# Kernel optimization log

Measured on AMD Instinct MI355X. Metric: run time of the kernel, lower is better.

Reference implementation:

```python
import jax, jax.numpy as jnp
import numpy as np

STRIDE = 1
PAD = 1

def setup_inputs() -> dict:
    key = jax.random.key(0)
    k1, k2 = jax.random.split(key)
    x = jax.random.normal(k1, (32, 128, 56, 56), dtype=jnp.float32)
    W = jax.random.normal(k2, (256, 128, 3, 3), dtype=jnp.float32)
    b = jnp.zeros((256,), dtype=jnp.float32)
    return {"x": x, "W": W, "b": b}

def reference(x, W, b):
    # Faithful conv2d: NCHW input, OIHW weight, stride 1, pad 1, plus bias.
    out = jax.lax.conv_general_dilated(
        x, W,
        window_strides=(STRIDE, STRIDE),
        padding=((PAD, PAD), (PAD, PAD)),
        dimension_numbers=("NCHW", "OIHW", "NCHW"),
    )
    return out + b[None, :, None, None]
```

## Files before the change

kernel.cpp:

```cpp
#include <hip/hip_runtime.h>
#include <hip/hip_bf16.h>
#include <cstdint>
#include <cstddef>

#define NB   32
#define CIN  128
#define HWP  3136
#define KOC  256
#define NRS  9
#define PSTR 58
#define PROW 3364
#define WIN  256
#define WINB (WIN * 64)

typedef __attribute__((ext_vector_type(8))) short  short8;
typedef __attribute__((ext_vector_type(4))) short  short4v;
typedef __attribute__((ext_vector_type(4))) float  float4v;

__device__ __forceinline__ unsigned short f2bf(float f) {
    union { float f; unsigned int u; } v; v.f = f;
    unsigned int u = v.u;
    u = u + 0x7fffu + ((u >> 16) & 1u);
    return (unsigned short)(u >> 16);
}

__global__ __launch_bounds__(256) void prep_kernel(const float* __restrict__ W,
                                                   unsigned short* __restrict__ wt2,
                                                   const float* __restrict__ x,
                                                   unsigned short* __restrict__ xt) {
    __shared__ unsigned short lds[32 * 260];
    int blk = blockIdx.x;
    int t   = threadIdx.x;

    if (blk < 1152) {
        int idx = blk * 256 + t;
        int e    = idx & 7;
        int lr   = (idx >> 3) & 15;
        int quad = (idx >> 7) & 3;
        int i    = (idx >> 9) & 3;
        int wm   = (idx >> 11) & 1;
        int ot   = (idx >> 12) & 1;
        int ck   = (idx >> 13) & 3;
        int rs   = idx >> 15;
        int oc = ot * 128 + wm * 64 + i * 16 + lr;
        int c  = ck * 32 + quad * 8 + e;
        wt2[idx] = f2bf(W[((size_t)oc * CIN + c) * NRS + rs]);
        return;
    }

    if (blk >= 2816) {
        int g = (blk - 2816) * 256 + t;
        int slab = g / 228;
        int gi   = g - slab * 228;
        int row;
        if (gi < 59)       row = gi;
        else if (gi < 169) { int k = gi - 59;
                             row = 115 + 58 * (k >> 1) + (k & 1); }
        else               row = 3305 + (gi - 169);
        unsigned short* gr = xt + (size_t)slab * (PROW * 32) + (size_t)row * 32;
        short8 z = (short8)0;
        *(short8*)(gr +  0) = z;
        *(short8*)(gr +  8) = z;
        *(short8*)(gr + 16) = z;
        *(short8*)(gr + 24) = z;
        return;
    }

    int b    = blk - 1152;
    int tile = b % 13;
    int ck   = (b / 13) & 3;
    int n    = b / 52;
    int hw0  = tile * 256;
    int wv   = t >> 6;
    int lane = t & 63;

    const float* src = x + ((size_t)(n * CIN + ck * 32)) * HWP;
    #pragma unroll
    for (int pass = 0; pass < 8; ++pass) {
        int c  = pass * 4 + wv;
        int hw = hw0 + lane * 4;
        if (hw < HWP) {
            float4v v = *(const float4v*)(src + (size_t)c * HWP + hw);
            short4v s4;
            #pragma unroll
            for (int k = 0; k < 4; ++k) s4[k] = (short)f2bf(v[k]);
            *(short4v*)(&lds[c * 260 + lane * 4]) = s4;
        }
    }
    __syncthreads();

    int sub = t & 3;
    int hwl = t >> 2;
    unsigned short* dst = xt + ((size_t)(n * 4 + ck)) * PROW * 32;
    #pragma unroll
    for (int pass = 0; pass < 4; ++pass) {
        int hl = pass * 64 + hwl;
        int hw = hw0 + hl;
        if (hw < HWP) {
            short8 v;
            #pragma unroll
            for (int j = 0; j < 8; ++j)
                v[j] = (short)lds[(sub * 8 + j) * 260 + hl];
            int pr = hw + 59 + 2 * (hw / 56);
            *(short8*)(dst + (size_t)pr * 32 + sub * 8) = v;
        }
    }
}

__device__ __forceinline__ void stage_window(const unsigned short* gwin,
                                             unsigned short* lwin,
                                             int wv, int lane) {
    #pragma unroll
    for (int it = 0; it < 4; ++it) {
        int blk = it * 4 + wv;
        int s   = blk * 64 + lane;
        int r   = s >> 2;
        int q   = s & 3;
        int qs  = q ^ ((r >> 1) & 3);
        const char* g = (const char*)gwin + r * 64 + qs * 16;
        char*       l = (char*)lwin + blk * 1024;
        __builtin_amdgcn_global_load_lds(
            (const __attribute__((address_space(1))) void*)g,
            (__attribute__((address_space(3))) void*)l, 16, 0, 0);
    }
}

__device__ __forceinline__ short8 ldb(const char* lb, int r, int quad) {
    int q = quad ^ ((r >> 1) & 3);
    return *(const short8*)(lb + r * 64 + q * 16);
}

__global__ __launch_bounds__(256, 4) void gemm_kernel(const unsigned short* __restrict__ xt,
                                                      const unsigned short* __restrict__ wt2,
                                                      const float* __restrict__ bias,
                                                      float* __restrict__ out) {
    __shared__ unsigned short b_lds[2 * WIN * 32];

    int bx  = blockIdx.x;
    int ot  = bx & 1;
    int n   = (bx >> 1) & 31;
    int pt  = bx >> 6;
    int oc0 = ot * 128;
    int p0  = pt * 128;

    int t    = threadIdx.x;
    int wv   = t >> 6;
    int lane = t & 63;
    int lr   = lane & 15;
    int quad = lane >> 4;
    int wm   = wv >> 1;
    int wn   = wv & 1;

    int prbase = p0 + 2 * (p0 / 56);

    int rb[4];
    #pragma unroll
    for (int j = 0; j < 4; ++j) {
        int hw  = p0 + wn * 64 + j * 16 + lr;
        int hwc = hw < HWP ? hw : (HWP - 1);
        rb[j] = hwc + 59 + 2 * (hwc / 56) - prbase;
    }

    const unsigned short* xb = xt + (size_t)n * 4 * PROW * 32;

    float4v acc[4][4];
    #pragma unroll
    for (int i = 0; i < 4; ++i)
        #pragma unroll
        for (int j = 0; j < 4; ++j)
            acc[i][j] = (float4v){0.f, 0.f, 0.f, 0.f};

    const unsigned short* ap = wt2 + (ot * 4096 + wm * 2048 + lane * 8);
    short8 afc[4];
    #pragma unroll
    for (int i = 0; i < 4; ++i) afc[i] = *(const short8*)(ap + i * 512);

    stage_window(xb + (size_t)prbase * 32, b_lds, wv, lane);

    const int SH[9] = {-59, -58, -57, -1, 0, 1, 57, 58, 59};

    for (int ck = 0; ck < 4; ++ck) {
        __syncthreads();
        if (ck < 3)
            stage_window(xb + (size_t)(ck + 1) * (PROW * 32) + (size_t)prbase * 32,
                         b_lds + ((ck + 1) & 1) * (WIN * 32), wv, lane);
        const char* lb = (const char*)b_lds + (ck & 1) * WINB;

        #pragma unroll
        for (int rs = 0; rs < 9; ++rs) {
            ap += (rs == 8) ? -253952 : 32768;
            short8 afn[4];
            #pragma unroll
            for (int i = 0; i < 4; ++i) afn[i] = *(const short8*)(ap + i * 512);
            short8 bcur = ldb(lb, rb[0] + SH[rs], quad);
            #pragma unroll
            for (int j = 0; j < 4; ++j) {
                short8 bnext;
                if (j < 3) bnext = ldb(lb, rb[j + 1] + SH[rs], quad);
                #pragma unroll
                for (int i = 0; i < 4; ++i)
                    acc[i][j] = __builtin_amdgcn_mfma_f32_16x16x32_bf16(
                        afc[i], bcur, acc[i][j], 0, 0, 0);
                if (j < 3) bcur = bnext;
            }
            #pragma unroll
            for (int i = 0; i < 4; ++i) afc[i] = afn[i];
        }
    }

    float* orow = out + (size_t)n * KOC * HWP;
    #pragma unroll
    for (int i = 0; i < 4; ++i) {
        #pragma unroll
        for (int r = 0; r < 4; ++r) {
            int oc = oc0 + wm * 64 + i * 16 + quad * 4 + r;
            float bi = bias[oc];
            #pragma unroll
            for (int j = 0; j < 4; ++j) {
                int hw = p0 + wn * 64 + j * 16 + lr;
                if (hw < HWP)
                    orow[(size_t)oc * HWP + hw] = acc[i][j][r] + bi;
            }
        }
    }
}

__global__ void naive_kernel(const float* __restrict__ x, const float* __restrict__ W,
                             const float* __restrict__ b, float* __restrict__ out) {
    size_t idx = (size_t)blockIdx.x * 256 + threadIdx.x;
    if (idx >= (size_t)NB * KOC * HWP) return;
    int w0 = (int)(idx % 56);
    int h0 = (int)((idx / 56) % 56);
    int k  = (int)((idx / HWP) % KOC);
    int n  = (int)(idx / ((size_t)HWP * KOC));
    float acc = b[k];
    for (int c = 0; c < CIN; ++c) {
        const float* xr = x + ((size_t)n * CIN + c) * HWP;
        const float* wr = W + ((size_t)k * CIN + c) * NRS;
        for (int r = 0; r < 3; ++r) {
            int h = h0 + r - 1;
            if ((unsigned)h >= 56u) continue;
            for (int s = 0; s < 3; ++s) {
                int w = w0 + s - 1;
                if ((unsigned)w >= 56u) continue;
                acc += xr[h * 56 + w] * wr[r * 3 + s];
            }
        }
    }
    out[idx] = acc;
}

extern "C" void kernel_launch(void* const* d_in, const int* in_sizes, int n_in,
                              void* d_out, int out_size, void* d_ws, size_t ws_size,
                              hipStream_t stream) {
    const float* x  = (const float*)d_in[0];
    const float* W  = (const float*)d_in[1];
    const float* b  = (const float*)d_in[2];
    float* out = (float*)d_out;

    const size_t wt_elems = (size_t)NRS * 4 * 2 * 2 * 4 * 4 * 16 * 8;
    const size_t xt_elems = (size_t)NB * 4 * PROW * 32 + WIN * 32;
    const size_t need = (wt_elems + xt_elems) * sizeof(unsigned short);

    if (ws_size < need) {
        size_t total = (size_t)NB * KOC * HWP;
        naive_kernel<<<(unsigned)((total + 255) / 256), 256, 0, stream>>>(x, W, b, out);
        return;
    }

    unsigned short* wt2 = (unsigned short*)d_ws;
    unsigned short* xt  = wt2 + wt_elems;

    prep_kernel<<<1152 + NB * 4 * 13 + 114, 256, 0, stream>>>(W, wt2, x, xt);
    gemm_kernel<<<1600, 256, 0, stream>>>(xt, wt2, b, out);
}
```

Before: 216.0 us.

## Stage weights through LDS and enlarge GEMM tile to 256 pixels with 8 waves

The implicit-GEMM conv kernel now uses 512-thread blocks covering 128 output channels by 256 pixels, with a larger 384-row input window in LDS. Weight fragments are double-buffered into LDS via global_load_lds, one filter row (three taps) per stage, instead of each wave loading them directly from global memory. The weight prep layout is reordered to match the per-row staging. The intent is to share weight traffic across more pixels and halve the block count, at the cost of more LDS (96 KB), a barrier per filter row, and lower occupancy.

```diff
diff --git a/kernel.cpp b/kernel.cpp
--- a/kernel.cpp
+++ b/kernel.cpp
@@ -8,10 +8,9 @@
 #define HWP  3136
 #define KOC  256
 #define NRS  9
-#define PSTR 58
 #define PROW 3364
-#define WIN  256
-#define WINB (WIN * 64)
+#define WINR 384
+#define AEL  12288
 
 typedef __attribute__((ext_vector_type(8))) short  short8;
 typedef __attribute__((ext_vector_type(4))) short  short4v;
@@ -33,15 +32,19 @@
     int t   = threadIdx.x;
 
     if (blk < 1152) {
-        int idx = blk * 256 + t;
+        int idx  = blk * 256 + t;
         int e    = idx & 7;
         int lr   = (idx >> 3) & 15;
         int quad = (idx >> 7) & 3;
         int i    = (idx >> 9) & 3;
         int wm   = (idx >> 11) & 1;
-        int ot   = (idx >> 12) & 1;
-        int ck   = (idx >> 13) & 3;
-        int rs   = idx >> 15;
+        int rem  = idx >> 12;
+        int s    = rem % 3;
+        int q    = rem / 3;
+        int ot   = q & 1;
+        int r    = (q >> 1) % 3;
+        int ck   = q / 6;
+        int rs   = r * 3 + s;
         int oc = ot * 128 + wm * 64 + i * 16 + lr;
         int c  = ck * 32 + quad * 8 + e;
         wt2[idx] = f2bf(W[((size_t)oc * CIN + c) * NRS + rs]);
@@ -107,21 +110,31 @@
     }
 }
 
-__device__ __forceinline__ void stage_window(const unsigned short* gwin,
-                                             unsigned short* lwin,
-                                             int wv, int lane) {
-    #pragma unroll
-    for (int it = 0; it < 4; ++it) {
-        int blk = it * 4 + wv;
+__device__ __forceinline__ void stage_A(const unsigned short* src,
+                                        unsigned short* lbase,
+                                        int wv, int lane) {
+    #pragma unroll
+    for (int it = 0; it < 3; ++it) {
+        int c0 = it * 512 + wv * 64;
+        __builtin_amdgcn_global_load_lds(
+            (const __attribute__((address_space(1))) void*)(src + (size_t)(c0 + lane) * 8),
+            (__attribute__((address_space(3))) void*)(lbase + (size_t)c0 * 8), 16, 0, 0);
+    }
+}
+
+__device__ __forceinline__ void stage_B(const unsigned short* gwin,
+                                        unsigned short* lbase,
+                                        int wv, int lane) {
+    #pragma unroll
+    for (int it = 0; it < 3; ++it) {
+        int blk = it * 8 + wv;
         int s   = blk * 64 + lane;
         int r   = s >> 2;
         int q   = s & 3;
         int qs  = q ^ ((r >> 1) & 3);
-        const char* g = (const char*)gwin + r * 64 + qs * 16;
-        char*       l = (char*)lwin + blk * 1024;
         __builtin_amdgcn_global_load_lds(
-            (const __attribute__((address_space(1))) void*)g,
-            (__attribute__((address_space(3))) void*)l, 16, 0, 0);
+            (const __attribute__((address_space(1))) void*)(gwin + r * 32 + qs * 8),
+            (__attribute__((address_space(3))) void*)(lbase + (size_t)blk * 512), 16, 0, 0);
     }
 }
 
@@ -130,26 +143,25 @@
     return *(const short8*)(lb + r * 64 + q * 16);
 }
 
-__global__ __launch_bounds__(256, 4) void gemm_kernel(const unsigned short* __restrict__ xt,
+__global__ __launch_bounds__(512, 2) void gemm_kernel(const unsigned short* __restrict__ xt,
                                                       const unsigned short* __restrict__ wt2,
                                                       const float* __restrict__ bias,
                                                       float* __restrict__ out) {
-    __shared__ unsigned short b_lds[2 * WIN * 32];
-
-    int bx  = blockIdx.x;
-    int ot  = bx & 1;
-    int n   = (bx >> 1) & 31;
-    int pt  = bx >> 6;
-    int oc0 = ot * 128;
-    int p0  = pt * 128;
+    __shared__ unsigned short lds[49152];
+
+    int bx = blockIdx.x;
+    int ot = bx & 1;
+    int n  = (bx >> 1) & 31;
+    int pt = bx >> 6;
+    int p0 = pt * 256;
 
     int t    = threadIdx.x;
     int wv   = t >> 6;
     int lane = t & 63;
     int lr   = lane & 15;
     int quad = lane >> 4;
-    int wm   = wv >> 1;
-    int wn   = wv & 1;
+    int wm   = wv >> 2;
+    int wn   = wv & 3;
 
     int prbase = p0 + 2 * (p0 / 56);
 
@@ -162,6 +174,7 @@
     }
 
     const unsigned short* xb = xt + (size_t)n * 4 * PROW * 32;
+    const unsigned short* wb = wt2 + ot * AEL;
 
     float4v acc[4][4];
     #pragma unroll
@@ -170,41 +183,47 @@
         for (int j = 0; j < 4; ++j)
             acc[i][j] = (float4v){0.f, 0.f, 0.f, 0.f};
 
-    const unsigned short* ap = wt2 + (ot * 4096 + wm * 2048 + lane * 8);
-    short8 afc[4];
-    #pragma unroll
-    for (int i = 0; i < 4; ++i) afc[i] = *(const short8*)(ap + i * 512);
-
-    stage_window(xb + (size_t)prbase * 32, b_lds, wv, lane);
-
-    const int SH[9] = {-59, -58, -57, -1, 0, 1, 57, 58, 59};
+    stage_A(wb, lds, wv, lane);
+    stage_B(xb + (size_t)prbase * 32, lds + 24576, wv, lane);
+    __syncthreads();
 
     for (int ck = 0; ck < 4; ++ck) {
-        __syncthreads();
-        if (ck < 3)
-            stage_window(xb + (size_t)(ck + 1) * (PROW * 32) + (size_t)prbase * 32,
-                         b_lds + ((ck + 1) & 1) * (WIN * 32), wv, lane);
-        const char* lb = (const char*)b_lds + (ck & 1) * WINB;
-
-        #pragma unroll
-        for (int rs = 0; rs < 9; ++rs) {
-            ap += (rs == 8) ? -253952 : 32768;
-            short8 afn[4];
-            #pragma unroll
-            for (int i = 0; i < 4; ++i) afn[i] = *(const short8*)(ap + i * 512);
-            short8 bcur = ldb(lb, rb[0] + SH[rs], quad);
-            #pragma unroll
-            for (int j = 0; j < 4; ++j) {
-                short8 bnext;
-                if (j < 3) bnext = ldb(lb, rb[j + 1] + SH[rs], quad);
+        for (int r = 0; r < 3; ++r) {
+            int g = ck * 3 + r;
+            if (g < 11) {
+                int r2  = (r == 2) ? 0 : r + 1;
+                int ck2 = (r == 2) ? ck + 1 : ck;
+                stage_A(wb + (size_t)ck2 * 73728 + (size_t)r2 * 24576,
+                        lds + ((g + 1) & 1) * AEL, wv, lane);
+            }
+            if (r == 2 && ck < 3)
+                stage_B(xb + (size_t)(ck + 1) * (PROW * 32) + (size_t)prbase * 32,
+                        lds + 24576 + ((ck + 1) & 1) * AEL, wv, lane);
+
+            const unsigned short* A = lds + (g & 1) * AEL + wm * 2048 + lane * 8;
+            const char* lbB = (const char*)(lds + 24576 + (ck & 1) * AEL);
+            int sh0 = (r - 1) * 58;
+
+            #pragma unroll
+            for (int s = 0; s < 3; ++s) {
+                int shift = sh0 + s - 1;
+                short8 af[4];
                 #pragma unroll
                 for (int i = 0; i < 4; ++i)
-                    acc[i][j] = __builtin_amdgcn_mfma_f32_16x16x32_bf16(
-                        afc[i], bcur, acc[i][j], 0, 0, 0);
-                if (j < 3) bcur = bnext;
-            }
-            #pragma unroll
-            for (int i = 0; i < 4; ++i) afc[i] = afn[i];
+                    af[i] = *(const short8*)(A + s * 4096 + i * 512);
+                short8 bcur = ldb(lbB, rb[0] + shift, quad);
+                #pragma unroll
+                for (int j = 0; j < 4; ++j) {
+                    short8 bnext;
+                    if (j < 3) bnext = ldb(lbB, rb[j + 1] + shift, quad);
+                    #pragma unroll
+                    for (int i = 0; i < 4; ++i)
+                        acc[i][j] = __builtin_amdgcn_mfma_f32_16x16x32_bf16(
+                            af[i], bcur, acc[i][j], 0, 0, 0);
+                    if (j < 3) bcur = bnext;
+                }
+            }
+            __syncthreads();
         }
     }
 
@@ -212,14 +231,14 @@
     #pragma unroll
     for (int i = 0; i < 4; ++i) {
         #pragma unroll
-        for (int r = 0; r < 4; ++r) {
-            int oc = oc0 + wm * 64 + i * 16 + quad * 4 + r;
+        for (int rr = 0; rr < 4; ++rr) {
+            int oc = ot * 128 + wm * 64 + i * 16 + quad * 4 + rr;
             float bi = bias[oc];
             #pragma unroll
             for (int j = 0; j < 4; ++j) {
                 int hw = p0 + wn * 64 + j * 16 + lr;
                 if (hw < HWP)
-                    orow[(size_t)oc * HWP + hw] = acc[i][j][r] + bi;
+                    orow[(size_t)oc * HWP + hw] = acc[i][j][rr] + bi;
             }
         }
     }
@@ -259,7 +278,7 @@
     float* out = (float*)d_out;
 
     const size_t wt_elems = (size_t)NRS * 4 * 2 * 2 * 4 * 4 * 16 * 8;
-    const size_t xt_elems = (size_t)NB * 4 * PROW * 32 + WIN * 32;
+    const size_t xt_elems = (size_t)NB * 4 * PROW * 32 + (size_t)WINR * 32;
     const size_t need = (wt_elems + xt_elems) * sizeof(unsigned short);
 
     if (ws_size < need) {
@@ -272,5 +291,5 @@
     unsigned short* xt  = wt2 + wt_elems;
 
     prep_kernel<<<1152 + NB * 4 * 13 + 114, 256, 0, stream>>>(W, wt2, x, xt);
-    gemm_kernel<<<1600, 256, 0, stream>>>(xt, wt2, b, out);
-}
+    gemm_kernel<<<13 * 32 * 2, 512, 0, stream>>>(xt, wt2, b, out);
+}
```

Measured after the change: 219.6 us. Within noise of the previous version (+1.7%).
